# Performance work log

Hardware: AMD Instinct MI355X
Metric: run time of the kernel (lower is better)

## Reference

```python
import jax, jax.numpy as jnp
import numpy as np

N = 20000
E = 320000
H = 4
IN_DIM = 2000
# (in_dim, per-head out channels, concat) for each GATConv layer
LAYER_DIMS = [(2000, 128, True), (512, 64, True), (256, 32, True), (128, 64, False)]
NEG_SLOPE = 0.2  # PyG GATConv LeakyReLU slope


def setup_inputs() -> dict:
    key = jax.random.key(0)
    ks = jax.random.split(key, 2 + 4 * len(LAYER_DIMS))
    inp = {
        "x": jax.random.normal(ks[0], (N, IN_DIM), dtype=jnp.float32),
        "edge_index": jax.random.randint(ks[1], (2, E), 0, N, dtype=jnp.int64),
    }
    for i, (din, c, concat) in enumerate(LAYER_DIMS):
        k0, k1, k2, _ = jax.random.split(ks[2 + i], 4)
        inp[f"W{i}"] = (jax.random.normal(k0, (din, H * c), dtype=jnp.float32)
                         * (1.0 / np.sqrt(din)).astype(np.float32))
        inp[f"as{i}"] = jax.random.normal(k1, (H, c), dtype=jnp.float32) * 0.1
        inp[f"ad{i}"] = jax.random.normal(k2, (H, c), dtype=jnp.float32) * 0.1
        inp[f"b{i}"] = jnp.zeros((H * c if concat else c,), dtype=jnp.float32)
    return inp


def gat_conv(x, src, dst, W, att_src, att_dst, bias, concat):
    n, c = x.shape[0], W.shape[1] // H
    h = (x @ W).reshape(n, H, c)                      # (N,H,C) per-head features
    a_s = jnp.einsum("nhc,hc->nh", h, att_src)        # (N,H) source logits
    a_d = jnp.einsum("nhc,hc->nh", h, att_dst)        # (N,H) target logits
    e = a_s[src] + a_d[dst]                           # (E,H) per-edge logits
    e = jnp.where(e > 0, e, NEG_SLOPE * e)            # leaky_relu
    # segment softmax over edges sharing the same target node
    m = jax.ops.segment_max(e, dst, num_segments=n)   # (N,H)
    ex = jnp.exp(e - m[dst])
    denom = jax.ops.segment_sum(ex, dst, num_segments=n)
    alpha = ex / denom[dst]                           # (E,H)
    # weighted scatter-aggregate of source features
    out = jax.ops.segment_sum(alpha[:, :, None] * h[src], dst, num_segments=n)  # (N,H,C)
    out = out.reshape(n, H * c) if concat else out.mean(axis=1)
    return out + bias


def reference(x, edge_index, W0, as0, ad0, b0, W1, as1, ad1, b1,
              W2, as2, ad2, b2, W3, as3, ad3, b3):
    loops = jnp.arange(N, dtype=edge_index.dtype)
    src = jnp.concatenate([edge_index[0], loops])     # add self-loops (PyG default)
    dst = jnp.concatenate([edge_index[1], loops])
    params = [(W0, as0, ad0, b0), (W1, as1, ad1, b1), (W2, as2, ad2, b2), (W3, as3, ad3, b3)]
    h = x
    for i, (W, a_s, a_d, b) in enumerate(params):
        concat = LAYER_DIMS[i][2]
        h = gat_conv(h, src, dst, W, a_s, a_d, b, concat)
        if i < len(params) - 1:
            h = jax.nn.elu(h)  # dropout inactive in eval mode
    return h
```

## Files before the change

### kernel.cpp

```cpp
#include <hip/hip_runtime.h>
#include <hip/hip_bf16.h>

#define GN 20000
#define GE 320000
#define GETOT (GE + GN)
#define GH 4
#define NROW 20096

typedef __attribute__((ext_vector_type(8))) _Float16 f16x8;
typedef __attribute__((ext_vector_type(4))) float f32x4;

__global__ void detect_dtype_kernel(const void* __restrict__ ei, int* __restrict__ flag) {
    if (threadIdx.x == 0 && blockIdx.x == 0) {
        const long long* p = (const long long*)ei;
        int ok = 1;
        for (int i = 0; i < 16; ++i) {
            long long v = p[i];
            if (v < 0 || v >= GN) ok = 0;
        }
        *flag = ok;
    }
}

__device__ __forceinline__ int load_idx(const void* ei, int is64, long long pos) {
    if (is64) return (int)((const long long*)ei)[pos];
    return ((const int*)ei)[pos];
}

__global__ void hist_kernel(const void* __restrict__ ei, const int* __restrict__ flagp,
                            int* __restrict__ counts) {
    int e = blockIdx.x * blockDim.x + threadIdx.x;
    if (e >= GETOT) return;
    int d;
    if (e < GE) d = load_idx(ei, *flagp, (long long)GE + e);
    else        d = e - GE;
    atomicAdd(&counts[d], 1);
}

__global__ __launch_bounds__(1024) void scan_kernel(const int* __restrict__ counts,
                                                    int* __restrict__ offsets,
                                                    int* __restrict__ cursor) {
    __shared__ int sh[1024];
    const int tid = threadIdx.x;
    constexpr int CH = 20;
    const int base = tid * CH;
    int loc[CH];
    int sum = 0;
#pragma unroll
    for (int i = 0; i < CH; ++i) {
        int idx = base + i;
        int v = (idx < GN) ? counts[idx] : 0;
        loc[i] = sum;
        sum += v;
    }
    sh[tid] = sum;
    __syncthreads();
    for (int o = 1; o < 1024; o <<= 1) {
        int t = (tid >= o) ? sh[tid - o] : 0;
        __syncthreads();
        sh[tid] += t;
        __syncthreads();
    }
    const int excl = tid ? sh[tid - 1] : 0;
#pragma unroll
    for (int i = 0; i < CH; ++i) {
        int idx = base + i;
        if (idx < GN) {
            int o = excl + loc[i];
            offsets[idx] = o;
            cursor[idx]  = o;
        }
    }
    if (tid == 1023) offsets[GN] = sh[1023];
}

__global__ void scatter_kernel(const void* __restrict__ ei, const int* __restrict__ flagp,
                               int* __restrict__ cursor, int* __restrict__ csr_src) {
    int e = blockIdx.x * blockDim.x + threadIdx.x;
    if (e >= GETOT) return;
    int s, d;
    if (e < GE) {
        int is64 = *flagp;
        s = load_idx(ei, is64, e);
        d = load_idx(ei, is64, (long long)GE + e);
    } else {
        s = d = e - GE;
    }
    int pos = atomicAdd(&cursor[d], 1);
    csr_src[pos] = s;
}

__device__ __forceinline__ float h2f(unsigned u) {
    unsigned short us = (unsigned short)u;
    _Float16 h;
    __builtin_memcpy(&h, &us, 2);
    return (float)h;
}
__device__ __forceinline__ unsigned short f2h_bits(float v) {
    _Float16 h = (_Float16)v;
    unsigned short us;
    __builtin_memcpy(&us, &h, 2);
    return us;
}

__global__ void convert_wt(const float* __restrict__ W,
                           _Float16* __restrict__ thi,
                           int K, int N, int Kpad) {
    __shared__ float tile[32][33];
    int kb = blockIdx.x * 32, nb = blockIdx.y * 32;
    for (int i = threadIdx.y; i < 32; i += 8) {
        int k = kb + i, n = nb + threadIdx.x;
        tile[i][threadIdx.x] = (k < K) ? W[(size_t)k * N + n] : 0.f;
    }
    __syncthreads();
    for (int i = threadIdx.y; i < 32; i += 8) {
        int n = nb + i, k = kb + threadIdx.x;
        thi[(size_t)n * Kpad + k] = (_Float16)tile[threadIdx.x][i];
    }
}

__device__ __forceinline__ int swz(int a) { return a ^ (((a >> 6) & 7) << 4); }
__device__ __forceinline__ int invswz(int p) {
    int b8 = (p >> 8) & 1, b7 = (p >> 7) & 1;
    int a6 = ((p >> 6) & 1) ^ b8;
    int a5 = ((p >> 5) & 1) ^ b7;
    int a4 = ((p >> 4) & 1) ^ a6;
    return (p & ~0x70) | (a4 << 4) | (a5 << 5) | (a6 << 6);
}
__device__ __forceinline__ int swzA32(int a) { return a ^ (((a >> 7) & 7) << 4); }

#define GLDS16(gsrc, ldst) __builtin_amdgcn_global_load_lds( \
    (const __attribute__((address_space(1))) void*)(gsrc),   \
    (__attribute__((address_space(3))) void*)(ldst), 16, 0, 0)

template <int MODE, int CD>
__global__ __launch_bounds__(256, MODE == 1 ? 3 : 4) void gemm_f16(
        const void* __restrict__ Ap, int lda, int K,
        const _Float16* __restrict__ Whi,
        int Kpad, void* __restrict__ Cp, int M, int N, int NC,
        const float* __restrict__ att_s, const float* __restrict__ att_d,
        float* __restrict__ a_s, float* __restrict__ a_d) {
    constexpr int BUFB = (MODE == 1) ? 24576 : 16384;
    constexpr int WOFF = (MODE == 1) ? 16384 : 8192;
    __shared__ char lds[2 * BUFB];
    const int tid = threadIdx.x;

    const int nwg = gridDim.x;
    const int q = nwg >> 3, r = nwg & 7;
    const int xcd = blockIdx.x & 7, sub = blockIdx.x >> 3;
    const int orig = (xcd < r ? xcd * (q + 1) : r * (q + 1) + (xcd - r) * q) + sub;
    const int brow = (orig / NC) * 128;
    const int bcol = (orig % NC) * 128;

    const int lane = tid & 63, wid = tid >> 6;
    const int wr = wid >> 1, wc = wid & 1;
    const int l4 = lane & 15, kg = lane >> 4;

    int row8[2], ecol[2];
#pragma unroll
    for (int p = 0; p < 2; ++p) {
        int a = invswz(p * 4096 + tid * 16);
        row8[p] = a >> 6;
        ecol[p] = (a & 63) >> 1;
    }
    int rB[2];
#pragma unroll
    for (int p = 0; p < 2; ++p) rB[p] = bcol + row8[p];

    int rA2[2];
    int rA4[4], eA4[4];
    if constexpr (MODE == 1) {
#pragma unroll
        for (int p = 0; p < 4; ++p) {
            int a = swzA32(p * 4096 + tid * 16);
            int rr = brow + (a >> 7);
            rA4[p] = rr < M ? rr : M - 1;
            eA4[p] = (a & 127) >> 2;
        }
    } else {
#pragma unroll
        for (int p = 0; p < 2; ++p) rA2[p] = brow + row8[p];
    }
    const float*    A32 = (const float*)Ap;
    const _Float16* Af  = (const _Float16*)Ap;

    auto STAGE = [&](int buf, int k0) {
        char* bb = lds + buf * BUFB;
        if constexpr (MODE == 1) {
#pragma unroll
            for (int p = 0; p < 4; ++p) {
                int kk = k0 + eA4[p];
                if (kk >= K) kk = 0;
                GLDS16(A32 + (size_t)rA4[p] * lda + kk, bb + p * 4096 + tid * 16);
            }
        } else {
#pragma unroll
            for (int p = 0; p < 2; ++p)
                GLDS16(Af + (size_t)rA2[p] * lda + k0 + ecol[p], bb + p * 4096 + tid * 16);
        }
#pragma unroll
        for (int p = 0; p < 2; ++p)
            GLDS16(Whi + (size_t)rB[p] * Kpad + k0 + ecol[p], bb + WOFF + p * 4096 + tid * 16);
    };

    int aoff[4], boff[4];
#pragma unroll
    for (int m = 0; m < 4; ++m) {
        int row = wr * 64 + m * 16 + l4;
        aoff[m] = (MODE == 1) ? swzA32(row * 128 + kg * 32) : swz(row * 64 + kg * 16);
        boff[m] = swz((wc * 64 + m * 16 + l4) * 64 + kg * 16);
    }

    f32x4 acc[4][4];
#pragma unroll
    for (int m = 0; m < 4; ++m)
#pragma unroll
        for (int n = 0; n < 4; ++n) acc[m][n] = (f32x4)(0.f);

    const int nk = Kpad / 32;
    STAGE(0, 0);

    for (int t = 0; t < nk; ++t) {
        if (t + 1 < nk) {
            STAGE((t + 1) & 1, (t + 1) * 32);
            if constexpr (MODE == 1)
                asm volatile("s_waitcnt vmcnt(6)" ::: "memory");
            else
                asm volatile("s_waitcnt vmcnt(4)" ::: "memory");
        } else {
            asm volatile("s_waitcnt vmcnt(0)" ::: "memory");
        }
        __builtin_amdgcn_s_barrier();
        __builtin_amdgcn_sched_barrier(0);

        char* bb = lds + (t & 1) * BUFB;
        f16x8 av[4], wh[4];
        if constexpr (MODE == 1) {
            f32x4 u0[4], u1[4];
#pragma unroll
            for (int m = 0; m < 4; ++m) {
                u0[m] = *(const f32x4*)(bb + aoff[m]);
                u1[m] = *(const f32x4*)(bb + (aoff[m] ^ 16));
            }
            __builtin_amdgcn_sched_barrier(0);
#pragma unroll
            for (int n = 0; n < 4; ++n)
                wh[n] = *(const f16x8*)(bb + WOFF + boff[n]);
            __builtin_amdgcn_sched_barrier(0);
            asm volatile("s_waitcnt lgkmcnt(4)" ::: "memory");
            __builtin_amdgcn_sched_barrier(0);
#pragma unroll
            for (int m = 0; m < 4; ++m) {
                av[m][0] = (_Float16)u0[m].x; av[m][1] = (_Float16)u0[m].y;
                av[m][2] = (_Float16)u0[m].z; av[m][3] = (_Float16)u0[m].w;
                av[m][4] = (_Float16)u1[m].x; av[m][5] = (_Float16)u1[m].y;
                av[m][6] = (_Float16)u1[m].z; av[m][7] = (_Float16)u1[m].w;
            }
        } else {
#pragma unroll
            for (int m = 0; m < 4; ++m) av[m] = *(const f16x8*)(bb + aoff[m]);
#pragma unroll
            for (int n = 0; n < 4; ++n) wh[n] = *(const f16x8*)(bb + WOFF + boff[n]);
        }
        asm volatile("s_waitcnt lgkmcnt(0)" ::: "memory");
        __builtin_amdgcn_sched_barrier(0);

#pragma unroll
        for (int m = 0; m < 4; ++m)
#pragma unroll
            for (int n = 0; n < 4; ++n)
                acc[m][n] = __builtin_amdgcn_mfma_f32_16x16x32_f16(av[m], wh[n], acc[m][n], 0, 0, 0);
        __builtin_amdgcn_s_barrier();
    }

    float atS[4], atD[4];
    int   hn[4];
#pragma unroll
    for (int n = 0; n < 4; ++n) {
        int gc = bcol + wc * 64 + n * 16 + l4;
        int hd = gc / CD;
        hn[n]  = hd;
        atS[n] = att_s[hd * CD + (gc - hd * CD)];
        atD[n] = att_d[hd * CD + (gc - hd * CD)];
    }

#pragma unroll
    for (int m = 0; m < 4; ++m) {
        int gr0 = brow + wr * 64 + m * 16 + (lane >> 4) * 4;
#pragma unroll
        for (int rr2 = 0; rr2 < 4; ++rr2) {
            int gr = gr0 + rr2;
            float v0 = acc[m][0][rr2], v1 = acc[m][1][rr2];
            float v2 = acc[m][2][rr2], v3 = acc[m][3][rr2];
            if (gr < M) {
                size_t ob = (size_t)gr * N + bcol + wc * 64 + l4;
                if constexpr (MODE == 2) {
                    float* C32 = (float*)Cp;
                    C32[ob] = v0; C32[ob + 16] = v1; C32[ob + 32] = v2; C32[ob + 48] = v3;
                } else {
                    _Float16* C16 = (_Float16*)Cp;
                    C16[ob] = (_Float16)v0; C16[ob + 16] = (_Float16)v1;
                    C16[ob + 32] = (_Float16)v2; C16[ob + 48] = (_Float16)v3;
                }
            }
            float ps0 = v0 * atS[0] + v1 * atS[1];
            float ps1 = v2 * atS[2] + v3 * atS[3];
            float pd0 = v0 * atD[0] + v1 * atD[1];
            float pd1 = v2 * atD[2] + v3 * atD[3];
#pragma unroll
            for (int o2 = 1; o2 < 16; o2 <<= 1) {
                ps0 += __shfl_xor(ps0, o2);
                ps1 += __shfl_xor(ps1, o2);
                pd0 += __shfl_xor(pd0, o2);
                pd1 += __shfl_xor(pd1, o2);
            }
            if (l4 == 0 && gr < M) {
                if (hn[0] == hn[2]) {
                    atomicAdd(&a_s[gr * GH + hn[0]], ps0 + ps1);
                    atomicAdd(&a_d[gr * GH + hn[0]], pd0 + pd1);
                } else {
                    atomicAdd(&a_s[gr * GH + hn[0]], ps0);
                    atomicAdd(&a_s[gr * GH + hn[2]], ps1);
                    atomicAdd(&a_d[gr * GH + hn[0]], pd0);
                    atomicAdd(&a_d[gr * GH + hn[2]], pd1);
                }
            }
        }
    }
}

template <int C, int CPT, int BLOCK>
__global__ __launch_bounds__(BLOCK) void gat_aggregate_f16(
        const unsigned short* __restrict__ hfeat,
        const float* __restrict__ a_s,
        const float* __restrict__ a_d,
        const int* __restrict__ offsets,
        const int* __restrict__ csr_src,
        const float* __restrict__ bias,
        unsigned short* __restrict__ of16) {
    constexpr int HC = GH * C;
    static_assert(BLOCK * CPT == HC, "coverage");
    const int n     = blockIdx.x;
    const int tid   = threadIdx.x;
    const int start = offsets[n];
    const int end   = offsets[n + 1];

    __shared__ float s_m[GH];
    __shared__ float s_den[GH];
    __shared__ int   s_src[64];
    __shared__ float s_al[GH][68];

    const float4 ad4 = *(const float4*)(a_d + n * GH);
    const float adh[GH] = {ad4.x, ad4.y, ad4.z, ad4.w};

    if (tid < 64) {
        float lmax[GH], lsum[GH];
#pragma unroll
        for (int h = 0; h < GH; ++h) lmax[h] = -1e30f;
        for (int e = start + tid; e < end; e += 64) {
            int s = csr_src[e];
            float4 as4 = *(const float4*)(a_s + s * GH);
            float l[GH] = {as4.x + adh[0], as4.y + adh[1], as4.z + adh[2], as4.w + adh[3]};
#pragma unroll
            for (int h = 0; h < GH; ++h) {
                float ll = l[h] > 0.f ? l[h] : 0.2f * l[h];
                lmax[h] = fmaxf(lmax[h], ll);
            }
        }
#pragma unroll
        for (int h = 0; h < GH; ++h)
#pragma unroll
            for (int o = 32; o; o >>= 1) lmax[h] = fmaxf(lmax[h], __shfl_xor(lmax[h], o));
#pragma unroll
        for (int h = 0; h < GH; ++h) lsum[h] = 0.f;
        for (int e = start + tid; e < end; e += 64) {
            int s = csr_src[e];
            float4 as4 = *(const float4*)(a_s + s * GH);
            float l[GH] = {as4.x + adh[0], as4.y + adh[1], as4.z + adh[2], as4.w + adh[3]};
#pragma unroll
            for (int h = 0; h < GH; ++h) {
                float ll = l[h] > 0.f ? l[h] : 0.2f * l[h];
                lsum[h] += __expf(ll - lmax[h]);
            }
        }
#pragma unroll
        for (int h = 0; h < GH; ++h)
#pragma unroll
            for (int o = 32; o; o >>= 1) lsum[h] += __shfl_xor(lsum[h], o);
        if (tid == 0) {
#pragma unroll
            for (int h = 0; h < GH; ++h) { s_m[h] = lmax[h]; s_den[h] = lsum[h]; }
        }
    }
    __syncthreads();

    float mm[GH], inv[GH];
#pragma unroll
    for (int h = 0; h < GH; ++h) { mm[h] = s_m[h]; inv[h] = 1.0f / s_den[h]; }

    const int ch0 = tid * CPT;
    const int hd  = ch0 / C;
    float acc[CPT];
#pragma unroll
    for (int j = 0; j < CPT; ++j) acc[j] = 0.f;

    for (int e0 = start; e0 < end; e0 += 64) {
        __syncthreads();
        if (tid < 64) {
            bool vld = (e0 + tid) < end;
            int s = vld ? csr_src[e0 + tid] : n;
            s_src[tid] = s;
            float4 as4 = *(const float4*)(a_s + s * GH);
            float l[GH] = {as4.x + adh[0], as4.y + adh[1], as4.z + adh[2], as4.w + adh[3]};
#pragma unroll
            for (int h = 0; h < GH; ++h) {
                float ll = l[h] > 0.f ? l[h] : 0.2f * l[h];
                s_al[h][tid] = vld ? __expf(ll - mm[h]) * inv[h] : 0.f;
            }
        }
        __syncthreads();
        int cnt = end - e0; if (cnt > 64) cnt = 64;
        int cnt4 = (cnt + 3) & ~3;
        for (int i = 0; i < cnt4; i += 4) {
            int4   ss = *(const int4*)&s_src[i];
            float4 aa = *(const float4*)&s_al[hd][i];
            if constexpr (CPT == 4) {
                uint2 v0 = ((const uint2*)(hfeat + (size_t)ss.x * HC))[tid];
                uint2 v1 = ((const uint2*)(hfeat + (size_t)ss.y * HC))[tid];
                uint2 v2 = ((const uint2*)(hfeat + (size_t)ss.z * HC))[tid];
                uint2 v3 = ((const uint2*)(hfeat + (size_t)ss.w * HC))[tid];
                acc[0] = fmaf(aa.x, h2f(v0.x & 0xffff), acc[0]);
                acc[1] = fmaf(aa.x, h2f(v0.x >> 16),    acc[1]);
                acc[2] = fmaf(aa.x, h2f(v0.y & 0xffff), acc[2]);
                acc[3] = fmaf(aa.x, h2f(v0.y >> 16),    acc[3]);
                acc[0] = fmaf(aa.y, h2f(v1.x & 0xffff), acc[0]);
                acc[1] = fmaf(aa.y, h2f(v1.x >> 16),    acc[1]);
                acc[2] = fmaf(aa.y, h2f(v1.y & 0xffff), acc[2]);
                acc[3] = fmaf(aa.y, h2f(v1.y >> 16),    acc[3]);
                acc[0] = fmaf(aa.z, h2f(v2.x & 0xffff), acc[0]);
                acc[1] = fmaf(aa.z, h2f(v2.x >> 16),    acc[1]);
                acc[2] = fmaf(aa.z, h2f(v2.y & 0xffff), acc[2]);
                acc[3] = fmaf(aa.z, h2f(v2.y >> 16),    acc[3]);
                acc[0] = fmaf(aa.w, h2f(v3.x & 0xffff), acc[0]);
                acc[1] = fmaf(aa.w, h2f(v3.x >> 16),    acc[1]);
                acc[2] = fmaf(aa.w, h2f(v3.y & 0xffff), acc[2]);
                acc[3] = fmaf(aa.w, h2f(v3.y >> 16),    acc[3]);
            } else {
                unsigned v0 = ((const unsigned*)(hfeat + (size_t)ss.x * HC))[tid];
                unsigned v1 = ((const unsigned*)(hfeat + (size_t)ss.y * HC))[tid];
                unsigned v2 = ((const unsigned*)(hfeat + (size_t)ss.z * HC))[tid];
                unsigned v3 = ((const unsigned*)(hfeat + (size_t)ss.w * HC))[tid];
                acc[0] = fmaf(aa.x, h2f(v0 & 0xffff), acc[0]);
                acc[1] = fmaf(aa.x, h2f(v0 >> 16),    acc[1]);
                acc[0] = fmaf(aa.y, h2f(v1 & 0xffff), acc[0]);
                acc[1] = fmaf(aa.y, h2f(v1 >> 16),    acc[1]);
                acc[0] = fmaf(aa.z, h2f(v2 & 0xffff), acc[0]);
                acc[1] = fmaf(aa.z, h2f(v2 >> 16),    acc[1]);
                acc[0] = fmaf(aa.w, h2f(v3 & 0xffff), acc[0]);
                acc[1] = fmaf(aa.w, h2f(v3 >> 16),    acc[1]);
            }
        }
    }

    unsigned short hs[CPT];
#pragma unroll
    for (int j = 0; j < CPT; ++j) {
        float v = acc[j] + bias[ch0 + j];
        v = v > 0.f ? v : expm1f(v);
        hs[j] = f2h_bits(v);
    }
    unsigned short* op = of16 + (size_t)n * HC + ch0;
    if constexpr (CPT == 4) {
        uint2 hw = make_uint2((unsigned)hs[0] | ((unsigned)hs[1] << 16),
                              (unsigned)hs[2] | ((unsigned)hs[3] << 16));
        *(uint2*)op = hw;
    } else {
        *(unsigned*)op = (unsigned)hs[0] | ((unsigned)hs[1] << 16);
    }
}

__global__ __launch_bounds__(128) void gat_aggregate_final(
        const float* __restrict__ hfeat,
        const float* __restrict__ a_s,
        const float* __restrict__ a_d,
        const int* __restrict__ offsets,
        const int* __restrict__ csr_src,
        const float* __restrict__ bias,
        float* __restrict__ outf) {
    constexpr int C = 64, HC = GH * C;
    const int n     = blockIdx.x;
    const int tid   = threadIdx.x;
    const int start = offsets[n];
    const int end   = offsets[n + 1];

    __shared__ float s_m[GH];
    __shared__ float s_den[GH];
    __shared__ int   s_src[64];
    __shared__ float s_al[GH][68];
    __shared__ float sacc[256];

    const float4 ad4 = *(const float4*)(a_d + n * GH);
    const float adh[GH] = {ad4.x, ad4.y, ad4.z, ad4.w};

    if (tid < 64) {
        float lmax[GH], lsum[GH];
#pragma unroll
        for (int h = 0; h < GH; ++h) lmax[h] = -1e30f;
        for (int e = start + tid; e < end; e += 64) {
            int s = csr_src[e];
            float4 as4 = *(const float4*)(a_s + s * GH);
            float l[GH] = {as4.x + adh[0], as4.y + adh[1], as4.z + adh[2], as4.w + adh[3]};
#pragma unroll
            for (int h = 0; h < GH; ++h) {
                float ll = l[h] > 0.f ? l[h] : 0.2f * l[h];
                lmax[h] = fmaxf(lmax[h], ll);
            }
        }
#pragma unroll
        for (int h = 0; h < GH; ++h)
#pragma unroll
            for (int o = 32; o; o >>= 1) lmax[h] = fmaxf(lmax[h], __shfl_xor(lmax[h], o));
#pragma unroll
        for (int h = 0; h < GH; ++h) lsum[h] = 0.f;
        for (int e = start + tid; e < end; e += 64) {
            int s = csr_src[e];
            float4 as4 = *(const float4*)(a_s + s * GH);
            float l[GH] = {as4.x + adh[0], as4.y + adh[1], as4.z + adh[2], as4.w + adh[3]};
#pragma unroll
            for (int h = 0; h < GH; ++h) {
                float ll = l[h] > 0.f ? l[h] : 0.2f * l[h];
                lsum[h] += __expf(ll - lmax[h]);
            }
        }
#pragma unroll
        for (int h = 0; h < GH; ++h)
#pragma unroll
            for (int o = 32; o; o >>= 1) lsum[h] += __shfl_xor(lsum[h], o);
        if (tid == 0) {
#pragma unroll
            for (int h = 0; h < GH; ++h) { s_m[h] = lmax[h]; s_den[h] = lsum[h]; }
        }
    }
    __syncthreads();

    float mm[GH], inv[GH];
#pragma unroll
    for (int h = 0; h < GH; ++h) { mm[h] = s_m[h]; inv[h] = 1.0f / s_den[h]; }

    const int hd = (2 * tid) / C;
    float2 acc = make_float2(0.f, 0.f);

    for (int e0 = start; e0 < end; e0 += 64) {
        __syncthreads();
        if (tid < 64) {
            bool vld = (e0 + tid) < end;
            int s = vld ? csr_src[e0 + tid] : n;
            s_src[tid] = s;
            float4 as4 = *(const float4*)(a_s + s * GH);
            float l[GH] = {as4.x + adh[0], as4.y + adh[1], as4.z + adh[2], as4.w + adh[3]};
#pragma unroll
            for (int h = 0; h < GH; ++h) {
                float ll = l[h] > 0.f ? l[h] : 0.2f * l[h];
                s_al[h][tid] = vld ? __expf(ll - mm[h]) * inv[h] : 0.f;
            }
        }
        __syncthreads();
        int cnt = end - e0; if (cnt > 64) cnt = 64;
        int cnt4 = (cnt + 3) & ~3;
        for (int i = 0; i < cnt4; i += 4) {
            int4   ss = *(const int4*)&s_src[i];
            float4 aa = *(const float4*)&s_al[hd][i];
            float2 v0 = ((const float2*)(hfeat + (size_t)ss.x * HC))[tid];
            float2 v1 = ((const float2*)(hfeat + (size_t)ss.y * HC))[tid];
            float2 v2 = ((const float2*)(hfeat + (size_t)ss.z * HC))[tid];
            float2 v3 = ((const float2*)(hfeat + (size_t)ss.w * HC))[tid];
            acc.x = fmaf(aa.x, v0.x, acc.x); acc.y = fmaf(aa.x, v0.y, acc.y);
            acc.x = fmaf(aa.y, v1.x, acc.x); acc.y = fmaf(aa.y, v1.y, acc.y);
            acc.x = fmaf(aa.z, v2.x, acc.x); acc.y = fmaf(aa.z, v2.y, acc.y);
            acc.x = fmaf(aa.w, v3.x, acc.x); acc.y = fmaf(aa.w, v3.y, acc.y);
        }
    }

    sacc[2 * tid]     = acc.x;
    sacc[2 * tid + 1] = acc.y;
    __syncthreads();
    if (tid < C) {
        float v = 0.f;
#pragma unroll
        for (int h = 0; h < GH; ++h) v += sacc[h * C + tid];
        outf[(size_t)n * C + tid] = v * (1.0f / GH) + bias[tid];
    }
}

extern "C" void kernel_launch(void* const* d_in, const int* in_sizes, int n_in,
                              void* d_out, int out_size, void* d_ws, size_t ws_size,
                              hipStream_t stream) {
    const float* x  = (const float*)d_in[0];
    const void*  ei = d_in[1];
    const float* W[4]  = {(const float*)d_in[2],  (const float*)d_in[6],
                          (const float*)d_in[10], (const float*)d_in[14]};
    const float* AS[4] = {(const float*)d_in[3],  (const float*)d_in[7],
                          (const float*)d_in[11], (const float*)d_in[15]};
    const float* AD[4] = {(const float*)d_in[4],  (const float*)d_in[8],
                          (const float*)d_in[12], (const float*)d_in[16]};
    const float* BI[4] = {(const float*)d_in[5],  (const float*)d_in[9],
                          (const float*)d_in[13], (const float*)d_in[17]};

    char*  w   = (char*)d_ws;
    size_t off = 0;
    auto alloc = [&](size_t b) -> char* {
        char* p = w + off;
        off += (b + 255) & ~(size_t)255;
        return p;
    };
    int*   flag    = (int*)alloc(4);
    int*   counts  = (int*)alloc((GN + 1) * sizeof(int));
    int*   offsets = (int*)alloc((GN + 1) * sizeof(int));
    int*   cursor  = (int*)alloc(GN * sizeof(int));
    int*   csr_src = (int*)alloc((size_t)GETOT * sizeof(int));
    float* attb    = (float*)alloc((size_t)8 * GN * GH * sizeof(float));
    float* aS[4], *aD[4];
    for (int i = 0; i < 4; ++i) {
        aS[i] = attb + (size_t)(2 * i)     * GN * GH;
        aD[i] = attb + (size_t)(2 * i + 1) * GN * GH;
    }
    unsigned short* hA = (unsigned short*)alloc((size_t)NROW * 512 * 2);
    unsigned short* hB = (unsigned short*)alloc((size_t)NROW * 512 * 2);
    float* hbuf    = (float*)alloc((size_t)NROW * 256 * sizeof(float));
    _Float16* wt   = (_Float16*)alloc((size_t)512 * 2016 * 2);
    (void)in_sizes; (void)n_in; (void)out_size; (void)ws_size;

    detect_dtype_kernel<<<1, 64, 0, stream>>>(ei, flag);
    hipMemsetAsync(counts, 0, (GN + 1) * sizeof(int), stream);
    hipMemsetAsync(attb, 0, (size_t)8 * GN * GH * sizeof(float), stream);
    int eblocks = (GETOT + 255) / 256;
    hist_kernel<<<eblocks, 256, 0, stream>>>(ei, flag, counts);
    scan_kernel<<<1, 1024, 0, stream>>>(counts, offsets, cursor);
    scatter_kernel<<<eblocks, 256, 0, stream>>>(ei, flag, cursor, csr_src);

    const dim3 tb(32, 8);
    const int NR = (GN + 127) / 128;

    convert_wt<<<dim3(2016 / 32, 512 / 32), tb, 0, stream>>>(W[0], wt, 2000, 512, 2016);
    gemm_f16<1, 128><<<NR * 4, 256, 0, stream>>>(x, 2000, 2000, wt, 2016, hA, GN, 512, 4,
                                                 AS[0], AD[0], aS[0], aD[0]);
    gat_aggregate_f16<128, 4, 128><<<GN, 128, 0, stream>>>(hA, aS[0], aD[0], offsets, csr_src,
                                                           BI[0], hB);
    convert_wt<<<dim3(512 / 32, 256 / 32), tb, 0, stream>>>(W[1], wt, 512, 256, 512);
    gemm_f16<0, 64><<<NR * 2, 256, 0, stream>>>(hB, 512, 512, wt, 512, hA, GN, 256, 2,
                                                AS[1], AD[1], aS[1], aD[1]);
    gat_aggregate_f16<64, 4, 64><<<GN, 64, 0, stream>>>(hA, aS[1], aD[1], offsets, csr_src,
                                                        BI[1], hB);
    convert_wt<<<dim3(256 / 32, 128 / 32), tb, 0, stream>>>(W[2], wt, 256, 128, 256);
    gemm_f16<0, 32><<<NR * 1, 256, 0, stream>>>(hB, 256, 256, wt, 256, hA, GN, 128, 1,
                                                AS[2], AD[2], aS[2], aD[2]);
    gat_aggregate_f16<32, 2, 64><<<GN, 64, 0, stream>>>(hA, aS[2], aD[2], offsets, csr_src,
                                                        BI[2], hB);
    convert_wt<<<dim3(128 / 32, 256 / 32), tb, 0, stream>>>(W[3], wt, 128, 256, 128);
    gemm_f16<2, 64><<<NR * 2, 256, 0, stream>>>(hB, 128, 128, wt, 128, hbuf, GN, 256, 2,
                                                AS[3], AD[3], aS[3], aD[3]);
    gat_aggregate_final<<<GN, 128, 0, stream>>>(hbuf, aS[3], aD[3], offsets, csr_src,
                                                BI[3], (float*)d_out);
}
```

Baseline: 398.3 us.

## Restructure GEMM k-loop to single barrier and store final-layer features in fp16

The GEMM main loop now waits for all outstanding loads, does one barrier, and only then issues the next stage's prefetch. This removes the trailing barrier per iteration but no longer overlaps the next global load with the wait. Separately, the last layer's GEMM writes fp16 features instead of fp32, and the final aggregation reads packed half pairs and converts them. This halves the gather traffic in that kernel at some cost in precision.

```diff
diff --git a/kernel.cpp b/kernel.cpp
--- a/kernel.cpp
+++ b/kernel.cpp
@@ -221,17 +221,10 @@
     STAGE(0, 0);
 
     for (int t = 0; t < nk; ++t) {
-        if (t + 1 < nk) {
-            STAGE((t + 1) & 1, (t + 1) * 32);
-            if constexpr (MODE == 1)
-                asm volatile("s_waitcnt vmcnt(6)" ::: "memory");
-            else
-                asm volatile("s_waitcnt vmcnt(4)" ::: "memory");
-        } else {
-            asm volatile("s_waitcnt vmcnt(0)" ::: "memory");
-        }
+        asm volatile("s_waitcnt vmcnt(0)" ::: "memory");
         __builtin_amdgcn_s_barrier();
         __builtin_amdgcn_sched_barrier(0);
+        if (t + 1 < nk) STAGE((t + 1) & 1, (t + 1) * 32);
 
         char* bb = lds + (t & 1) * BUFB;
         f16x8 av[4], wh[4];
@@ -270,7 +263,6 @@
 #pragma unroll
             for (int n = 0; n < 4; ++n)
                 acc[m][n] = __builtin_amdgcn_mfma_f32_16x16x32_f16(av[m], wh[n], acc[m][n], 0, 0, 0);
-        __builtin_amdgcn_s_barrier();
     }
 
     float atS[4], atD[4];
@@ -294,14 +286,9 @@
             float v2 = acc[m][2][rr2], v3 = acc[m][3][rr2];
             if (gr < M) {
                 size_t ob = (size_t)gr * N + bcol + wc * 64 + l4;
-                if constexpr (MODE == 2) {
-                    float* C32 = (float*)Cp;
-                    C32[ob] = v0; C32[ob + 16] = v1; C32[ob + 32] = v2; C32[ob + 48] = v3;
-                } else {
-                    _Float16* C16 = (_Float16*)Cp;
-                    C16[ob] = (_Float16)v0; C16[ob + 16] = (_Float16)v1;
-                    C16[ob + 32] = (_Float16)v2; C16[ob + 48] = (_Float16)v3;
-                }
+                _Float16* C16 = (_Float16*)Cp;
+                C16[ob] = (_Float16)v0; C16[ob + 16] = (_Float16)v1;
+                C16[ob + 32] = (_Float16)v2; C16[ob + 48] = (_Float16)v3;
             }
             float ps0 = v0 * atS[0] + v1 * atS[1];
             float ps1 = v2 * atS[2] + v3 * atS[3];
@@ -479,8 +466,8 @@
     }
 }
 
-__global__ __launch_bounds__(128) void gat_aggregate_final(
-        const float* __restrict__ hfeat,
+__global__ __launch_bounds__(128) void gat_aggregate_final_f16(
+        const unsigned short* __restrict__ hfeat,
         const float* __restrict__ a_s,
         const float* __restrict__ a_d,
         const int* __restrict__ offsets,
@@ -548,7 +535,7 @@
     for (int h = 0; h < GH; ++h) { mm[h] = s_m[h]; inv[h] = 1.0f / s_den[h]; }
 
     const int hd = (2 * tid) / C;
-    float2 acc = make_float2(0.f, 0.f);
+    float acc0 = 0.f, acc1 = 0.f;
 
     for (int e0 = start; e0 < end; e0 += 64) {
         __syncthreads();
@@ -570,19 +557,23 @@
         for (int i = 0; i < cnt4; i += 4) {
             int4   ss = *(const int4*)&s_src[i];
             float4 aa = *(const float4*)&s_al[hd][i];
-            float2 v0 = ((const float2*)(hfeat + (size_t)ss.x * HC))[tid];
-            float2 v1 = ((const float2*)(hfeat + (size_t)ss.y * HC))[tid];
-            float2 v2 = ((const float2*)(hfeat + (size_t)ss.z * HC))[tid];
-            float2 v3 = ((const float2*)(hfeat + (size_t)ss.w * HC))[tid];
-            acc.x = fmaf(aa.x, v0.x, acc.x); acc.y = fmaf(aa.x, v0.y, acc.y);
-            acc.x = fmaf(aa.y, v1.x, acc.x); acc.y = fmaf(aa.y, v1.y, acc.y);
-            acc.x = fmaf(aa.z, v2.x, acc.x); acc.y = fmaf(aa.z, v2.y, acc.y);
-            acc.x = fmaf(aa.w, v3.x, acc.x); acc.y = fmaf(aa.w, v3.y, acc.y);
-        }
-    }
-
-    sacc[2 * tid]     = acc.x;
-    sacc[2 * tid + 1] = acc.y;
+            unsigned v0 = ((const unsigned*)(hfeat + (size_t)ss.x * HC))[tid];
+            unsigned v1 = ((const unsigned*)(hfeat + (size_t)ss.y * HC))[tid];
+            unsigned v2 = ((const unsigned*)(hfeat + (size_t)ss.z * HC))[tid];
+            unsigned v3 = ((const unsigned*)(hfeat + (size_t)ss.w * HC))[tid];
+            acc0 = fmaf(aa.x, h2f(v0 & 0xffff), acc0);
+            acc1 = fmaf(aa.x, h2f(v0 >> 16),    acc1);
+            acc0 = fmaf(aa.y, h2f(v1 & 0xffff), acc0);
+            acc1 = fmaf(aa.y, h2f(v1 >> 16),    acc1);
+            acc0 = fmaf(aa.z, h2f(v2 & 0xffff), acc0);
+            acc1 = fmaf(aa.z, h2f(v2 >> 16),    acc1);
+            acc0 = fmaf(aa.w, h2f(v3 & 0xffff), acc0);
+            acc1 = fmaf(aa.w, h2f(v3 >> 16),    acc1);
+        }
+    }
+
+    sacc[2 * tid]     = acc0;
+    sacc[2 * tid + 1] = acc1;
     __syncthreads();
     if (tid < C) {
         float v = 0.f;
@@ -626,7 +617,6 @@
     }
     unsigned short* hA = (unsigned short*)alloc((size_t)NROW * 512 * 2);
     unsigned short* hB = (unsigned short*)alloc((size_t)NROW * 512 * 2);
-    float* hbuf    = (float*)alloc((size_t)NROW * 256 * sizeof(float));
     _Float16* wt   = (_Float16*)alloc((size_t)512 * 2016 * 2);
     (void)in_sizes; (void)n_in; (void)out_size; (void)ws_size;
 
@@ -657,8 +647,8 @@
     gat_aggregate_f16<32, 2, 64><<<GN, 64, 0, stream>>>(hA, aS[2], aD[2], offsets, csr_src,
                                                         BI[2], hB);
     convert_wt<<<dim3(128 / 32, 256 / 32), tb, 0, stream>>>(W[3], wt, 128, 256, 128);
-    gemm_f16<2, 64><<<NR * 2, 256, 0, stream>>>(hB, 128, 128, wt, 128, hbuf, GN, 256, 2,
+    gemm_f16<0, 64><<<NR * 2, 256, 0, stream>>>(hB, 128, 128, wt, 128, hA, GN, 256, 2,
                                                 AS[3], AD[3], aS[3], aD[3]);
-    gat_aggregate_final<<<GN, 128, 0, stream>>>(hbuf, aS[3], aD[3], offsets, csr_src,
-                                                BI[3], (float*)d_out);
-}
+    gat_aggregate_final_f16<<<GN, 128, 0, stream>>>(hA, aS[3], aD[3], offsets, csr_src,
+                                                    BI[3], (float*)d_out);
+}
```

Measured after the change: 384.0 us. 1.04x faster.
